# Performance work log

Hardware: AMD Instinct MI355X
Metric: run time of the kernel (lower is better)

Reference implementation:

```python
import jax, jax.numpy as jnp
import numpy as np

MAX_DISP = 48


def setup_inputs() -> dict:
    key = jax.random.key(0)
    k1, k2 = jax.random.split(key)
    n, c, h, w = 2, 32, 136, 240
    left = jax.random.normal(k1, (n, c, h, w), dtype=jnp.float32)
    right = jax.random.normal(k2, (n, c, h, w), dtype=jnp.float32)
    return {"left": left, "right": right}


def _cost_volume(left, right, max_disp):
    # volume[n, c, d, h, w] = left[n,c,h,w] * right[n,c,h,w-d] for w >= d, else 0
    w = left.shape[-1]
    slices = []
    for d in range(max_disp):
        # shift right feature map by d along W, zero-padding on the left;
        # the zero pad makes volume[..., :d] zero automatically, matching the
        # torch loop that only writes volume[:, :, d, :, d:].
        shifted = jnp.pad(right, ((0, 0), (0, 0), (0, 0), (d, 0)))[..., :w]
        slices.append(left * shifted)
    return jnp.stack(slices, axis=2)  # N x C x D x H x W


def reference(left, right):
    return _cost_volume(left, right, MAX_DISP)
```

## Files before the change

kernel.cpp:

```cpp
#include <hip/hip_runtime.h>


constexpr int W    = 240;
constexpr int H    = 136;
constexpr int D    = 48;
constexpr int W4   = W / 4;
constexpr int PAD  = D;
constexpr int PAD4 = PAD / 4;
constexpr int CLEN = PAD + W;

typedef float v4f __attribute__((ext_vector_type(4)));

__global__ __launch_bounds__(256) void cost_volume_kernel(
    const float* __restrict__ left,
    const float* __restrict__ right,
    float* __restrict__ out)
{
    __shared__ __align__(16) float sC[4][CLEN];

    const int h    = blockIdx.x;
    const int nc   = blockIdx.y;
    const int tid  = threadIdx.x;
    const int wave = tid >> 6;
    const int lane = tid & 63;
    const size_t row = (size_t)(nc * H + h) * W;

    v4f l4 = (v4f){0.f, 0.f, 0.f, 0.f};
    if (lane < W4) l4 = reinterpret_cast<const v4f*>(left + row)[lane];

    for (int y = tid; y < 4 * CLEN; y += 256) {
        const int j = y / CLEN;
        const int x = y - j * CLEN;
        const int r = x - PAD - j;
        sC[j][x] = (r >= 0) ? right[row + r] : 0.0f;
    }
    __syncthreads();

    if (lane >= W4) return;

    const v4f* C0 = reinterpret_cast<const v4f*>(sC[0]);
    const v4f* C1 = reinterpret_cast<const v4f*>(sC[1]);
    const v4f* C2 = reinterpret_cast<const v4f*>(sC[2]);
    const v4f* C3 = reinterpret_cast<const v4f*>(sC[3]);

    const int d0 = wave * (D / 4);
    v4f* out4 = reinterpret_cast<v4f*>(out)
              + (((size_t)nc * D + d0) * H + h) * (size_t)W4 + lane;
    const size_t ds4 = (size_t)H * W4;

    #pragma unroll
    for (int tt = 0; tt < 3; ++tt) {
        const int q    = 3 * wave + tt;
        const int base = PAD4 + lane - q;
        const v4f r0 = C0[base];
        const v4f r1 = C1[base];
        const v4f r2 = C2[base];
        const v4f r3 = C3[base];
        v4f* o = out4 + (size_t)(4 * tt) * ds4;
        o[0]        = l4 * r0;
        o[ds4]      = l4 * r1;
        o[2 * ds4]  = l4 * r2;
        o[3 * ds4]  = l4 * r3;
    }
}

extern "C" void kernel_launch(void* const* d_in, const int* in_sizes, int n_in,
                              void* d_out, int out_size, void* d_ws, size_t ws_size,
                              hipStream_t stream) {
    const float* left  = (const float*)d_in[0];
    const float* right = (const float*)d_in[1];
    float* out = (float*)d_out;
    const int rows = in_sizes[0] / W;
    const int nc   = rows / H;
    dim3 grid(H, nc);
    cost_volume_kernel<<<grid, 256, 0, stream>>>(left, right, out);
}
```

Measured before the change: 421.0 us.

## Process four rows per block with each thread covering all disparities

Each block now handles four H rows. Left and shifted right rows for all four are staged in shared memory, and each thread writes all 48 disparity slices for its column instead of a quarter of them. This cuts block count and per-block staging overhead and gives each thread more independent stores. In exchange it uses more shared memory per block and launches fewer blocks, which may reduce occupancy and latency hiding.

```diff
diff --git a/kernel.cpp b/kernel.cpp
--- a/kernel.cpp
+++ b/kernel.cpp
@@ -5,9 +5,11 @@
 constexpr int H    = 136;
 constexpr int D    = 48;
 constexpr int W4   = W / 4;
+constexpr int ROWS = 4;
+constexpr int NT   = H / ROWS;
 constexpr int PAD  = D;
-constexpr int PAD4 = PAD / 4;
 constexpr int CLEN = PAD + W;
+constexpr int RTOT = 4 * ROWS * CLEN;
 
 typedef float v4f __attribute__((ext_vector_type(4)));
 
@@ -16,51 +18,59 @@
     const float* __restrict__ right,
     float* __restrict__ out)
 {
-    __shared__ __align__(16) float sC[4][CLEN];
+    __shared__ __align__(16) float sL[ROWS * W];
+    __shared__ __align__(16) float sR[4][ROWS][CLEN];
 
-    const int h    = blockIdx.x;
-    const int nc   = blockIdx.y;
-    const int tid  = threadIdx.x;
-    const int wave = tid >> 6;
-    const int lane = tid & 63;
-    const size_t row = (size_t)(nc * H + h) * W;
+    const int ht  = blockIdx.x;
+    const int nc  = blockIdx.y;
+    const int h0  = ht * ROWS;
+    const int tid = threadIdx.x;
 
-    v4f l4 = (v4f){0.f, 0.f, 0.f, 0.f};
-    if (lane < W4) l4 = reinterpret_cast<const v4f*>(left + row)[lane];
+    const float* __restrict__ Lg = left  + (size_t)(nc * H + h0) * W;
+    const float* __restrict__ Rg = right + (size_t)(nc * H + h0) * W;
 
-    for (int y = tid; y < 4 * CLEN; y += 256) {
-        const int j = y / CLEN;
-        const int x = y - j * CLEN;
-        const int r = x - PAD - j;
-        sC[j][x] = (r >= 0) ? right[row + r] : 0.0f;
+    if (tid < ROWS * W4) {
+        reinterpret_cast<v4f*>(sL)[tid] =
+            reinterpret_cast<const v4f*>(Lg)[tid];
+    }
+    for (int y = tid; y < RTOT; y += 256) {
+        const int j   = y / (ROWS * CLEN);
+        const int rem = y - j * (ROWS * CLEN);
+        const int r   = rem / CLEN;
+        const int x   = rem - r * CLEN;
+        const int src = x - PAD - j;
+        sR[0][0][y] = (src >= 0) ? Rg[r * W + src] : 0.0f;
     }
     __syncthreads();
 
-    if (lane >= W4) return;
+    if (tid >= ROWS * W4) return;
 
-    const v4f* C0 = reinterpret_cast<const v4f*>(sC[0]);
-    const v4f* C1 = reinterpret_cast<const v4f*>(sC[1]);
-    const v4f* C2 = reinterpret_cast<const v4f*>(sC[2]);
-    const v4f* C3 = reinterpret_cast<const v4f*>(sC[3]);
+    const int r  = tid / W4;
+    const int w4 = tid - r * W4;
 
-    const int d0 = wave * (D / 4);
-    v4f* out4 = reinterpret_cast<v4f*>(out)
-              + (((size_t)nc * D + d0) * H + h) * (size_t)W4 + lane;
+    const v4f l4 = reinterpret_cast<const v4f*>(sL)[tid];
+
+    v4f* __restrict__ o = reinterpret_cast<v4f*>(out)
+        + ((size_t)nc * D * H + (h0 + r)) * (size_t)W4 + w4;
     const size_t ds4 = (size_t)H * W4;
 
+    const v4f* C0 = reinterpret_cast<const v4f*>(sR[0][r]);
+    const v4f* C1 = reinterpret_cast<const v4f*>(sR[1][r]);
+    const v4f* C2 = reinterpret_cast<const v4f*>(sR[2][r]);
+    const v4f* C3 = reinterpret_cast<const v4f*>(sR[3][r]);
+
     #pragma unroll
-    for (int tt = 0; tt < 3; ++tt) {
-        const int q    = 3 * wave + tt;
-        const int base = PAD4 + lane - q;
+    for (int q = 0; q < D / 4; ++q) {
+        const int base = w4 + PAD / 4 - q;
         const v4f r0 = C0[base];
         const v4f r1 = C1[base];
         const v4f r2 = C2[base];
         const v4f r3 = C3[base];
-        v4f* o = out4 + (size_t)(4 * tt) * ds4;
-        o[0]        = l4 * r0;
-        o[ds4]      = l4 * r1;
-        o[2 * ds4]  = l4 * r2;
-        o[3 * ds4]  = l4 * r3;
+        v4f* oq = o + (size_t)(4 * q) * ds4;
+        oq[0]       = l4 * r0;
+        oq[ds4]     = l4 * r1;
+        oq[2 * ds4] = l4 * r2;
+        oq[3 * ds4] = l4 * r3;
     }
 }
 
@@ -72,6 +82,6 @@
     float* out = (float*)d_out;
     const int rows = in_sizes[0] / W;
     const int nc   = rows / H;
-    dim3 grid(H, nc);
+    dim3 grid(NT, nc);
     cost_volume_kernel<<<grid, 256, 0, stream>>>(left, right, out);
 }
```

New measurement: 409.9 us. 2.6% less time.
